# Kernel optimization log

Hardware: AMD Instinct MI355X
Metric: run time of the kernel (lower is better)

## Reference

```python
import jax, jax.numpy as jnp
import numpy as np

NUM_HEADS = 32
NUM_KV_HEADS = 8
HEAD_DIM = 128
GROUPS = NUM_HEADS // NUM_KV_HEADS  # 4
ROPE_BASE = 1000000.0


def _rope_cos_sin(seq_len, dtype):
    inv_freq = 1.0 / (ROPE_BASE ** (jnp.arange(0, HEAD_DIM, 2, dtype=jnp.float32) / HEAD_DIM))
    t = jnp.arange(seq_len, dtype=jnp.float32)
    freqs = jnp.einsum('i,j->ij', t, inv_freq)          # [S, D/2]
    emb = jnp.concatenate([freqs, freqs], axis=-1)       # [S, D]
    return jnp.cos(emb).astype(dtype), jnp.sin(emb).astype(dtype)


def _rotate_half(x):
    x1, x2 = jnp.split(x, 2, axis=-1)
    return jnp.concatenate([-x2, x1], axis=-1)


def setup_inputs() -> dict:
    key = jax.random.key(0)
    k1, k2, k3 = jax.random.split(key, 3)
    B, S, H = 1, 2048, 4096
    hidden_states = jax.random.normal(k1, (B, S, H), dtype=jnp.float32)
    wqkv = jax.random.normal(k2, (6144, H), dtype=jnp.float32) * (H ** -0.5)
    wo = jax.random.normal(k3, (H, H), dtype=jnp.float32) * (H ** -0.5)
    # causal additive mask [B, 1, S, S]
    neg = jnp.finfo(jnp.float32).min
    causal = jnp.triu(jnp.full((S, S), neg, dtype=jnp.float32), k=1)
    attention_mask = causal[None, None]
    position_ids = jnp.broadcast_to(jnp.arange(S, dtype=jnp.int64 if jax.config.jax_enable_x64 else jnp.int32), (B, S))
    return {'hidden_states': hidden_states, 'wqkv': wqkv, 'wo': wo,
            'attention_mask': attention_mask, 'position_ids': position_ids}


def reference(hidden_states, wqkv, wo, attention_mask, position_ids):
    B, S, _ = hidden_states.shape
    qkv = hidden_states @ wqkv.T                               # [B, S, 6144]
    qkv = qkv.reshape(B, S, NUM_KV_HEADS, GROUPS + 2, HEAD_DIM)
    q = qkv[..., :GROUPS, :].reshape(B, S, NUM_HEADS, HEAD_DIM)
    k = qkv[..., -2, :]                                        # [B, S, KVH, D]
    v = qkv[..., -1, :]
    q = q.transpose(0, 2, 1, 3)                                # [B, H, S, D]
    k = k.transpose(0, 2, 1, 3)                                # [B, KVH, S, D]
    v = v.transpose(0, 2, 1, 3)

    cos, sin = _rope_cos_sin(S, hidden_states.dtype)
    cos = cos[position_ids][:, None]                           # [B, 1, S, D]
    sin = sin[position_ids][:, None]
    q = q * cos + _rotate_half(q) * sin
    k = k * cos + _rotate_half(k) * sin

    # repeat_kv: [B, KVH, S, D] -> [B, H, S, D]
    k = jnp.repeat(k, GROUPS, axis=1)
    v = jnp.repeat(v, GROUPS, axis=1)

    scale = 1.0 / jnp.sqrt(jnp.asarray(HEAD_DIM, dtype=q.dtype))
    scores = jnp.einsum('bhqd,bhkd->bhqk', q, k) * scale + attention_mask
    probs = jax.nn.softmax(scores.astype(jnp.float32), axis=-1).astype(q.dtype)
    attn = jnp.einsum('bhqk,bhkd->bhqd', probs, v)             # [B, H, S, D]
    attn = attn.transpose(0, 2, 1, 3).reshape(B, S, NUM_HEADS * HEAD_DIM)
    return attn @ wo.T
```

## Files before the change

kernel.cpp:

```cpp
#include <hip/hip_runtime.h>
#include <stdint.h>

typedef unsigned short u16;
typedef unsigned int u32;
typedef short s16x8 __attribute__((ext_vector_type(8)));
typedef __bf16 bfv8 __attribute__((ext_vector_type(8)));
typedef float f32x4 __attribute__((ext_vector_type(4)));

#define S_LEN 2048
#define HID 4096
#define NQKV 6144

#define MFMA16(d, a, b) (d) = __builtin_amdgcn_mfma_f32_16x16x32_bf16((a), (b), (d), 0, 0, 0)

__device__ __forceinline__ u16 f2bf(float f){
  u32 u = __float_as_uint(f);
  return (u16)((u + 0x7fffu + ((u >> 16) & 1u)) >> 16);
}
__device__ __forceinline__ float bf2f(u16 x){
  return __uint_as_float((u32)x << 16);
}

__device__ __forceinline__ void gl16(const u16* g, u16* l){
  __builtin_amdgcn_global_load_lds((const __attribute__((address_space(1))) u32*)g,
                                   (__attribute__((address_space(3))) u32*)l,
                                   16, 0, 0);
}

__global__ __launch_bounds__(256) void cvt_bf16(const float* __restrict__ in,
                                                u16* __restrict__ out, int n4){
  int i = blockIdx.x * 256 + threadIdx.x;
  if (i >= n4) return;
  float4 v = ((const float4*)in)[i];
  ushort4 o;
  o.x = f2bf(v.x); o.y = f2bf(v.y); o.z = f2bf(v.z); o.w = f2bf(v.w);
  ((ushort4*)out)[i] = o;
}

template<typename OT>
__global__ __launch_bounds__(256) void gemm_bt(const u16* __restrict__ A,
                                               const u16* __restrict__ B,
                                               OT* __restrict__ C, int N, int K){
  __shared__ __align__(16) u16 As[2][128*32];
  __shared__ __align__(16) u16 Bs[2][128*32];
  const int tid = threadIdx.x;
  const int lane = tid & 63, wave = tid >> 6;
  const int g = lane >> 4, l16 = lane & 15;
  const int wr = wave >> 1, wc = wave & 1;
  const u16* Ag = A + (size_t)blockIdx.y * 128 * K;
  const u16* Bg = B + (size_t)blockIdx.x * 128 * K;
  const int r0 = wave*32 + (lane >> 2);
  const int r1 = r0 + 16;
  const int su = lane & 3;
  const int l0 = wave*1024;
  const int l1 = wave*1024 + 512;
  f32x4 acc[4][4] = {};

#define ISSUE(b, k0)                                          \
  gl16(Ag + (size_t)r0*K + (k0) + su*8, &As[b][l0]);          \
  gl16(Ag + (size_t)r1*K + (k0) + su*8, &As[b][l1]);          \
  gl16(Bg + (size_t)r0*K + (k0) + su*8, &Bs[b][l0]);          \
  gl16(Bg + (size_t)r1*K + (k0) + su*8, &Bs[b][l1]);

  ISSUE(0, 0)
  __syncthreads();
  const int KIT = K >> 5;
  for (int it = 0; it < KIT; it++){
    const int b = it & 1;
    if (it + 1 < KIT){ ISSUE(b^1, (it+1)*32) }
    bfv8 af[4], bfr[4];
    #pragma unroll
    for (int i = 0; i < 4; i++)
      af[i] = *(const bfv8*)&As[b][(wr*64 + i*16 + l16)*32 + g*8];
    #pragma unroll
    for (int j = 0; j < 4; j++)
      bfr[j] = *(const bfv8*)&Bs[b][(wc*64 + j*16 + l16)*32 + g*8];
    #pragma unroll
    for (int i = 0; i < 4; i++)
      #pragma unroll
      for (int j = 0; j < 4; j++)
        MFMA16(acc[i][j], af[i], bfr[j]);
    __syncthreads();
  }
#undef ISSUE
  OT* Cp = C + (size_t)(blockIdx.y*128 + wr*64) * N + blockIdx.x*128 + wc*64;
  #pragma unroll
  for (int i = 0; i < 4; i++)
    #pragma unroll
    for (int j = 0; j < 4; j++)
      #pragma unroll
      for (int r = 0; r < 4; r++){
        float v = acc[i][j][r];
        if constexpr (sizeof(OT) == 2)
          Cp[(size_t)(i*16 + g*4 + r) * N + j*16 + l16] = f2bf(v);
        else
          Cp[(size_t)(i*16 + g*4 + r) * N + j*16 + l16] = v;
      }
}

__global__ __launch_bounds__(256) void rope_reorg(const u16* __restrict__ qkv,
                                                  const int* __restrict__ pos,
                                                  u16* __restrict__ Qb, u16* __restrict__ Kb){
  const int hh = blockIdx.x;
  const int s  = blockIdx.y*4 + (threadIdx.x >> 6);
  const int j  = threadIdx.x & 63;
  const float p = (float)pos[s];
  const float inv = __expf(-(float)j * (13.815510557964274f / 64.0f));
  float sn, cs;
  sincosf(p * inv, &sn, &cs);
  const u16* src;
  u16* dst;
  if (hh < 32){
    src = qkv + (size_t)s*NQKV + (hh >> 2)*768 + (hh & 3)*128;
    dst = Qb + ((size_t)hh*S_LEN + s)*128;
  } else {
    int h = hh - 32;
    src = qkv + (size_t)s*NQKV + h*768 + 512;
    dst = Kb + ((size_t)h*S_LEN + s)*128;
  }
  float x1 = bf2f(src[j]), x2 = bf2f(src[j + 64]);
  dst[j]      = f2bf(x1*cs - x2*sn);
  dst[j + 64] = f2bf(x2*cs + x1*sn);
}

__global__ __launch_bounds__(256) void v_transpose(const u16* __restrict__ qkv,
                                                   u16* __restrict__ Vt){
  __shared__ u16 T[64][72];
  const int st = blockIdx.x, dt = blockIdx.y, h = blockIdx.z;
  const int w = threadIdx.x >> 6, lane = threadIdx.x & 63;
  const int s0 = st*64, d0 = dt*64;
  #pragma unroll
  for (int i = 0; i < 16; i++){
    int sl = w*16 + i;
    T[sl][lane] = qkv[(size_t)(s0+sl)*NQKV + h*768 + 640 + d0 + lane];
  }
  __syncthreads();
  #pragma unroll
  for (int i = 0; i < 16; i++){
    int dl = w*16 + i;
    Vt[((size_t)h*128 + d0 + dl)*S_LEN + s0 + lane] = T[lane][dl];
  }
}

__global__ __launch_bounds__(256) void attn_fwd(const u16* __restrict__ Q,
                                                const u16* __restrict__ K,
                                                const u16* __restrict__ V,
                                                u16* __restrict__ O){
  __shared__ __align__(16) u16 Ks[64*128];
  __shared__ __align__(16) u16 Vs[128*64];
  __shared__ __align__(16) u16 Ps[4][16][72];
  const int hq = blockIdx.x;
  const int qblk = 31 - blockIdx.y;
  const int hk = hq >> 2;
  const int tid = threadIdx.x, lane = tid & 63, w = tid >> 6;
  const int g = lane >> 4, l16 = lane & 15;
  const int q0 = qblk*64 + w*16;
  const u16* Qg = Q + ((size_t)hq*S_LEN + q0 + l16)*128;
  bfv8 qf[4];
  #pragma unroll
  for (int kk = 0; kk < 4; kk++) qf[kk] = *(const bfv8*)(Qg + kk*32 + g*8);
  const u16* Kg = K + (size_t)hk*S_LEN*128;
  const u16* Vg = V + (size_t)hk*128*S_LEN;
  f32x4 oacc[8] = {};
  float m_run[4], l_run[4];
  #pragma unroll
  for (int r = 0; r < 4; r++){ m_run[r] = -1e30f; l_run[r] = 0.0f; }
  const float scale = 0.08838834764831845f;

  const int rowk = w*16 + (lane >> 4);
  const int rowv = w*32 + (lane >> 3);

#define KV_LOAD(t, kr, vr)                                                        \
  _Pragma("unroll")                                                               \
  for (int i = 0; i < 4; i++){                                                    \
    kr[i] = *(const s16x8*)(Kg + ((size_t)((t)*64 + rowk + i*4))*128 + (lane & 15)*8); \
    vr[i] = *(const s16x8*)(Vg + (size_t)(rowv + i*8)*S_LEN + (t)*64 + (lane & 7)*8);  \
  }
#define KV_STORE(kr, vr)                                                          \
  _Pragma("unroll")                                                               \
  for (int i = 0; i < 4; i++){                                                    \
    int rk = rowk + i*4, rv = rowv + i*8;                                         \
    *(s16x8*)&Ks[rk*128 + ((lane & 15) ^ (rk & 7))*8] = kr[i];                    \
    *(s16x8*)&Vs[rv*64  + ((lane & 7)  ^ (rv & 7))*8] = vr[i];                    \
  }

  {
    s16x8 kr[4], vr[4];
    KV_LOAD(0, kr, vr)
    KV_STORE(kr, vr)
  }
  __syncthreads();

  for (int t = 0; t <= qblk; t++){
    s16x8 nkr[4], nvr[4];
    if (t + 1 <= qblk){ KV_LOAD(t+1, nkr, nvr) }
    f32x4 sacc[4] = {};
    #pragma unroll
    for (int j = 0; j < 4; j++){
      int row = j*16 + l16;
      #pragma unroll
      for (int kk = 0; kk < 4; kk++){
        bfv8 kf = *(const bfv8*)&Ks[row*128 + ((kk*4 + g) ^ (row & 7))*8];
        MFMA16(sacc[j], qf[kk], kf);
      }
    }
    float sc[4][4];
    #pragma unroll
    for (int j = 0; j < 4; j++)
      #pragma unroll
      for (int r = 0; r < 4; r++)
        sc[j][r] = sacc[j][r] * scale;
    if (t == qblk){
      #pragma unroll
      for (int j = 0; j < 4; j++){
        int kvc = t*64 + j*16 + l16;
        #pragma unroll
        for (int r = 0; r < 4; r++)
          if (kvc > q0 + g*4 + r) sc[j][r] = -1e30f;
      }
    }
    float mx[4];
    #pragma unroll
    for (int r = 0; r < 4; r++)
      mx[r] = fmaxf(fmaxf(sc[0][r], sc[1][r]), fmaxf(sc[2][r], sc[3][r]));
    #pragma unroll
    for (int off = 1; off < 16; off <<= 1)
      #pragma unroll
      for (int r = 0; r < 4; r++)
        mx[r] = fmaxf(mx[r], __shfl_xor(mx[r], off));
    float sf[4], pr[4][4], rsum[4];
    #pragma unroll
    for (int r = 0; r < 4; r++){
      float mn = fmaxf(m_run[r], mx[r]);
      sf[r] = __expf(m_run[r] - mn);
      m_run[r] = mn;
    }
    #pragma unroll
    for (int j = 0; j < 4; j++)
      #pragma unroll
      for (int r = 0; r < 4; r++)
        pr[j][r] = __expf(sc[j][r] - m_run[r]);
    #pragma unroll
    for (int r = 0; r < 4; r++)
      rsum[r] = (pr[0][r] + pr[1][r]) + (pr[2][r] + pr[3][r]);
    #pragma unroll
    for (int off = 1; off < 16; off <<= 1)
      #pragma unroll
      for (int r = 0; r < 4; r++)
        rsum[r] += __shfl_xor(rsum[r], off);
    #pragma unroll
    for (int r = 0; r < 4; r++)
      l_run[r] = l_run[r]*sf[r] + rsum[r];
    #pragma unroll
    for (int n = 0; n < 8; n++)
      #pragma unroll
      for (int r = 0; r < 4; r++)
        oacc[n][r] *= sf[r];
    #pragma unroll
    for (int j = 0; j < 4; j++)
      #pragma unroll
      for (int r = 0; r < 4; r++)
        Ps[w][g*4 + r][j*16 + l16] = f2bf(pr[j][r]);
    bfv8 pf[2];
    #pragma unroll
    for (int kk = 0; kk < 2; kk++)
      pf[kk] = *(const bfv8*)&Ps[w][l16][kk*32 + g*8];
    #pragma unroll
    for (int n = 0; n < 8; n++){
      int drow = n*16 + l16;
      #pragma unroll
      for (int kk = 0; kk < 2; kk++){
        bfv8 vf = *(const bfv8*)&Vs[drow*64 + ((kk*4 + g) ^ (drow & 7))*8];
        MFMA16(oacc[n], pf[kk], vf);
      }
    }
    __syncthreads();
    if (t + 1 <= qblk){ KV_STORE(nkr, nvr) }
    __syncthreads();
  }
#undef KV_LOAD
#undef KV_STORE
  #pragma unroll
  for (int r = 0; r < 4; r++){
    float invl = 1.0f / l_run[r];
    #pragma unroll
    for (int n = 0; n < 8; n++)
      O[(size_t)(q0 + g*4 + r)*HID + hq*128 + n*16 + l16] = f2bf(oacc[n][r]*invl);
  }
}

extern "C" void kernel_launch(void* const* d_in, const int* in_sizes, int n_in,
                              void* d_out, int out_size, void* d_ws, size_t ws_size,
                              hipStream_t stream){
  const float* hidden = (const float*)d_in[0];
  const float* wqkv   = (const float*)d_in[1];
  const float* wo     = (const float*)d_in[2];
  const int*   pos    = (const int*)d_in[4];
  float* out = (float*)d_out;
  char* ws = (char*)d_ws;

  u16* hB    = (u16*)(ws);
  u16* wqkvB = (u16*)(ws + (16ull<<20));
  u16* woB   = (u16*)(ws + (16ull<<20));
  u16* qkvB  = (u16*)(ws + (64ull<<20));
  u16* attnB = (u16*)(ws + (64ull<<20));
  u16* Qb    = (u16*)(ws + (88ull<<20));
  u16* Kb    = (u16*)(ws + (104ull<<20));
  u16* Vtb   = (u16*)(ws + (108ull<<20));

  cvt_bf16<<<dim3(8192),  256, 0, stream>>>(hidden, hB, 2097152);
  cvt_bf16<<<dim3(24576), 256, 0, stream>>>(wqkv, wqkvB, 6291456);
  gemm_bt<u16><<<dim3(48,16), 256, 0, stream>>>(hB, wqkvB, qkvB, NQKV, HID);
  cvt_bf16<<<dim3(16384), 256, 0, stream>>>(wo, woB, 4194304);
  rope_reorg<<<dim3(40,512), 256, 0, stream>>>(qkvB, pos, Qb, Kb);
  v_transpose<<<dim3(32,2,8), 256, 0, stream>>>(qkvB, Vtb);
  attn_fwd<<<dim3(32,32), 256, 0, stream>>>(Qb, Kb, Vtb, attnB);
  gemm_bt<float><<<dim3(32,16), 256, 0, stream>>>(attnB, woB, out, HID, HID);
}
```

Measured before the change: 542.0 us.

## Double-buffer K via async global-to-LDS loads and read V directly from global

K tiles are now prefetched with global_load_lds into a double-buffered LDS array, so the next tile streams in while the current one is computed. The register staging and one of the two barriers per iteration are removed. V is no longer staged in LDS; its MFMA fragments are loaded straight from global memory, where the transposed layout gives contiguous 16-byte reads. This lowers LDS traffic and synchronisation, but V now comes through L2/global with latency exposed inside the PV loop.

```diff
diff --git a/kernel.cpp b/kernel.cpp
--- a/kernel.cpp
+++ b/kernel.cpp
@@ -146,8 +146,7 @@
                                                 const u16* __restrict__ K,
                                                 const u16* __restrict__ V,
                                                 u16* __restrict__ O){
-  __shared__ __align__(16) u16 Ks[64*128];
-  __shared__ __align__(16) u16 Vs[128*64];
+  __shared__ __align__(16) u16 Ks[2][64*128];
   __shared__ __align__(16) u16 Ps[4][16][72];
   const int hq = blockIdx.x;
   const int qblk = 31 - blockIdx.y;
@@ -167,40 +166,28 @@
   for (int r = 0; r < 4; r++){ m_run[r] = -1e30f; l_run[r] = 0.0f; }
   const float scale = 0.08838834764831845f;
 
-  const int rowk = w*16 + (lane >> 4);
-  const int rowv = w*32 + (lane >> 3);
-
-#define KV_LOAD(t, kr, vr)                                                        \
+  const int krow = w*4 + (lane >> 4);
+  const int ksrc = ((lane & 15) ^ (krow & 7));
+
+#define ISSUE_K(t, b)                                                             \
   _Pragma("unroll")                                                               \
-  for (int i = 0; i < 4; i++){                                                    \
-    kr[i] = *(const s16x8*)(Kg + ((size_t)((t)*64 + rowk + i*4))*128 + (lane & 15)*8); \
-    vr[i] = *(const s16x8*)(Vg + (size_t)(rowv + i*8)*S_LEN + (t)*64 + (lane & 7)*8);  \
-  }
-#define KV_STORE(kr, vr)                                                          \
-  _Pragma("unroll")                                                               \
-  for (int i = 0; i < 4; i++){                                                    \
-    int rk = rowk + i*4, rv = rowv + i*8;                                         \
-    *(s16x8*)&Ks[rk*128 + ((lane & 15) ^ (rk & 7))*8] = kr[i];                    \
-    *(s16x8*)&Vs[rv*64  + ((lane & 7)  ^ (rv & 7))*8] = vr[i];                    \
-  }
-
-  {
-    s16x8 kr[4], vr[4];
-    KV_LOAD(0, kr, vr)
-    KV_STORE(kr, vr)
-  }
+  for (int i = 0; i < 4; i++)                                                     \
+    gl16(Kg + ((size_t)((t)*64 + i*16 + krow))*128 + ksrc*8,                      \
+         &Ks[b][(i*16 + w*4)*128]);
+
+  ISSUE_K(0, 0)
   __syncthreads();
 
   for (int t = 0; t <= qblk; t++){
-    s16x8 nkr[4], nvr[4];
-    if (t + 1 <= qblk){ KV_LOAD(t+1, nkr, nvr) }
+    const int b = t & 1;
+    if (t < qblk){ ISSUE_K(t+1, b^1) }
     f32x4 sacc[4] = {};
     #pragma unroll
     for (int j = 0; j < 4; j++){
       int row = j*16 + l16;
       #pragma unroll
       for (int kk = 0; kk < 4; kk++){
-        bfv8 kf = *(const bfv8*)&Ks[row*128 + ((kk*4 + g) ^ (row & 7))*8];
+        bfv8 kf = *(const bfv8*)&Ks[b][row*128 + ((kk*4 + g) ^ (row & 7))*8];
         MFMA16(sacc[j], qf[kk], kf);
       }
     }
@@ -270,16 +257,13 @@
       int drow = n*16 + l16;
       #pragma unroll
       for (int kk = 0; kk < 2; kk++){
-        bfv8 vf = *(const bfv8*)&Vs[drow*64 + ((kk*4 + g) ^ (drow & 7))*8];
+        bfv8 vf = *(const bfv8*)(Vg + (size_t)drow*S_LEN + t*64 + kk*32 + g*8);
         MFMA16(oacc[n], pf[kk], vf);
       }
     }
     __syncthreads();
-    if (t + 1 <= qblk){ KV_STORE(nkr, nvr) }
-    __syncthreads();
-  }
-#undef KV_LOAD
-#undef KV_STORE
+  }
+#undef ISSUE_K
   #pragma unroll
   for (int r = 0; r < 4; r++){
     float invl = 1.0f / l_run[r];
```

New measurement: 622.3 us. 1.15x slower.
